# Kernel optimization log

Hardware: AMD Instinct MI355X
Metric: run time of the kernel (lower is better)

## Reference

```python
import jax, jax.numpy as jnp
import numpy as np

N_TRAIN, D, B, N_CLASSES, K = 50000, 64, 128, 10, 16


def setup_inputs() -> dict:
    key = jax.random.key(0)
    k1, k2, k3 = jax.random.split(key, 3)
    train_data = jax.random.normal(k1, (N_TRAIN, D), dtype=jnp.float32)
    # one-hot class labels, as implied by gather -> sum over k -> argmax over classes
    labels = jax.random.randint(k2, (N_TRAIN,), 0, N_CLASSES)
    train_target = jax.nn.one_hot(labels, N_CLASSES, dtype=jnp.float32)
    x_test = jax.random.normal(k3, (B, D), dtype=jnp.float32)
    return {"train_data": train_data, "train_target": train_target,
            "x_test": x_test, "k": K}


def reference(train_data, train_target, x_test, k):
    # L1 (Manhattan) distance: [B, N_train]
    # broadcast: [1, N, D] - [B, 1, D] -> abs -> sum over D
    distance = jnp.sum(jnp.abs(train_data[None, :, :] - x_test[:, None, :]), axis=2)
    # top_k of negative distance == k nearest neighbors
    _, top_k_indices = jax.lax.top_k(-distance, k)          # [B, k]
    top_k_label = train_target[top_k_indices]               # [B, k, C] gather
    sum_up_predictions = jnp.sum(top_k_label, axis=1)       # [B, C] vote counts
    return jnp.argmax(sum_up_predictions, axis=1)           # [B] predicted class
```

## Files before the change

kernel.cpp:

```cpp
#include <hip/hip_runtime.h>
#include <cfloat>
#include <climits>
#include <stdint.h>

#define NTRAIN 50000
#define DIM 64
#define BQ 128
#define NCLS 10
#define KSEL 16
#define QPB 32
#define QG (BQ / QPB)
#define THREADS 512
#define TROWS 512
#define TPAD 68
#define NSAMP 1024
#define SSTRIPES 64
#define MARGIN 1e-2f

__device__ __forceinline__ uint64_t pack_di(float d, int r) {
    return ((uint64_t)__float_as_uint(d) << 32) | (uint32_t)r;
}

__device__ __forceinline__ void ins16(uint64_t (&K)[KSEL], uint64_t pk) {
    if (pk < K[KSEL - 1]) {
        K[KSEL - 1] = pk;
#pragma unroll
        for (int j = KSEL - 1; j > 0; --j)
            if (K[j] < K[j - 1]) { uint64_t t = K[j]; K[j] = K[j - 1]; K[j - 1] = t; }
    }
}

__device__ __forceinline__ uint64_t adv16(const uint64_t (&K)[KSEL], int c) {
    uint64_t nh = ~0ULL;
#pragma unroll
    for (int q = 1; q < KSEL; ++q)
        if (c == q) nh = K[q];
    return nh;
}

__device__ __forceinline__ void wave_merge8(const uint64_t (&K)[KSEL], int rg, uint64_t* dst) {
    uint64_t h = K[0]; int c = 0;
#pragma unroll
    for (int r = 0; r < KSEL; ++r) {
        uint64_t m = h, o;
        o = __shfl_xor((unsigned long long)m, 1); if (o < m) m = o;
        o = __shfl_xor((unsigned long long)m, 2); if (o < m) m = o;
        o = __shfl_xor((unsigned long long)m, 4); if (o < m) m = o;
        if (m == h) { ++c; h = adv16(K, c); }
        if (rg == (r & 7)) dst[r] = m;
    }
}

__global__ __launch_bounds__(64) void knn_tau(
    const float* __restrict__ train, const float* __restrict__ xtest,
    float* __restrict__ tau)
{
    const int q = blockIdx.x, lane = threadIdx.x;

    float4 qv[DIM / 4];
    {
        const float* qp = xtest + (size_t)q * DIM;
#pragma unroll
        for (int c = 0; c < DIM / 4; ++c) qv[c] = *(const float4*)(qp + 4 * c);
    }

    uint64_t K[KSEL];
#pragma unroll
    for (int j = 0; j < KSEL; ++j) K[j] = ~0ULL;

    for (int t = 0; t < NSAMP / 64; ++t) {
        const int r = lane + 64 * t;
        const float* rp = train + (size_t)r * DIM;
        float acc = 0.0f;
#pragma unroll
        for (int c = 0; c < DIM / 4; ++c) {
            const float4 tv = *(const float4*)(rp + 4 * c);
            const float s01 = fabsf(tv.x - qv[c].x) + fabsf(tv.y - qv[c].y);
            const float s23 = fabsf(tv.z - qv[c].z) + fabsf(tv.w - qv[c].w);
            acc += s01 + s23;
        }
        ins16(K, pack_di(acc, r));
    }

    uint64_t h = K[0]; int c = 0; uint64_t last = ~0ULL;
#pragma unroll
    for (int r = 0; r < KSEL; ++r) {
        uint64_t m = h, o;
#pragma unroll
        for (int sh = 1; sh < 64; sh <<= 1) {
            o = __shfl_xor((unsigned long long)m, sh);
            if (o < m) m = o;
        }
        if (m == h) { ++c; h = adv16(K, c); }
        last = m;
    }
    if (lane == 0) tau[q] = __uint_as_float((uint32_t)(last >> 32)) + MARGIN;
}

__global__ __launch_bounds__(THREADS, 2) void knn_scan(
    const float* __restrict__ train, const float* __restrict__ xtest,
    const float* __restrict__ tau, uint64_t* __restrict__ cand, int stripe_len)
{
    __shared__ float qs[QPB * TPAD];
    __shared__ __align__(16) float ts[TROWS * TPAD];

    const int bx     = blockIdx.x;
    const int stripe = bx % SSTRIPES;
    const int qgrp   = bx / SSTRIPES;
    const int q0     = qgrp * QPB;
    const int tid    = threadIdx.x;
    const int w      = tid >> 6;
    const int lane   = tid & 63;
    const int qg     = lane >> 3;
    const int rg     = lane & 7;

    const int r0 = stripe * stripe_len;
    const int r1 = min(NTRAIN, r0 + stripe_len);

    for (int f = tid; f < QPB * (DIM / 4); f += THREADS) {
        const int ql = f >> 4, c = f & 15;
        *(float4*)&qs[ql * TPAD + 4 * c] =
            *(const float4*)&xtest[(size_t)(q0 + ql) * DIM + 4 * c];
    }

    float tauv[4];
#pragma unroll
    for (int i = 0; i < 4; ++i) tauv[i] = tau[q0 + qg + 8 * i];

    uint64_t k0[KSEL], k1[KSEL], k2[KSEL], k3[KSEL];
#pragma unroll
    for (int j = 0; j < KSEL; ++j) { k0[j] = ~0ULL; k1[j] = ~0ULL; k2[j] = ~0ULL; k3[j] = ~0ULL; }

    for (int base = r0; base < r1; base += TROWS) {
        const int nr = min(TROWS, r1 - base);
        __syncthreads();
        for (int f = tid; f < nr * (DIM / 4); f += THREADS) {
            const int r = f >> 4, c = f & 15;
            *(float4*)&ts[r * TPAD + 4 * c] =
                *(const float4*)&train[(size_t)(base + r) * DIM + 4 * c];
        }
        __syncthreads();

        float acc[4][8];
#pragma unroll
        for (int i = 0; i < 4; ++i)
#pragma unroll
            for (int j = 0; j < 8; ++j) acc[i][j] = 0.0f;

#pragma unroll 4
        for (int c = 0; c < DIM / 4; ++c) {
            float4 qv[4], tv[8];
#pragma unroll
            for (int i = 0; i < 4; ++i)
                qv[i] = *(const float4*)&qs[(qg + 8 * i) * TPAD + 4 * c];
#pragma unroll
            for (int j = 0; j < 8; ++j)
                tv[j] = *(const float4*)&ts[(w * 64 + rg + 8 * j) * TPAD + 4 * c];
#pragma unroll
            for (int i = 0; i < 4; ++i)
#pragma unroll
                for (int j = 0; j < 8; ++j) {
                    const float s01 = fabsf(tv[j].x - qv[i].x) + fabsf(tv[j].y - qv[i].y);
                    const float s23 = fabsf(tv[j].z - qv[i].z) + fabsf(tv[j].w - qv[i].w);
                    acc[i][j] += s01 + s23;
                }
        }

        const int rb = base + w * 64 + rg;
#pragma unroll
        for (int j = 0; j < 8; ++j) {
            const int r = rb + 8 * j;
            if (r < r1) {
                if (acc[0][j] <= tauv[0]) ins16(k0, pack_di(acc[0][j], r));
                if (acc[1][j] <= tauv[1]) ins16(k1, pack_di(acc[1][j], r));
                if (acc[2][j] <= tauv[2]) ins16(k2, pack_di(acc[2][j], r));
                if (acc[3][j] <= tauv[3]) ins16(k3, pack_di(acc[3][j], r));
            }
        }
    }

    __syncthreads();
    uint64_t* mg = (uint64_t*)ts;
    wave_merge8(k0, rg, &mg[((size_t)w * QPB + qg +  0) * 17]);
    wave_merge8(k1, rg, &mg[((size_t)w * QPB + qg +  8) * 17]);
    wave_merge8(k2, rg, &mg[((size_t)w * QPB + qg + 16) * 17]);
    wave_merge8(k3, rg, &mg[((size_t)w * QPB + qg + 24) * 17]);
    __syncthreads();

    if (tid < QPB) {
        uint64_t kk[KSEL];
#pragma unroll
        for (int j = 0; j < KSEL; ++j) kk[j] = ~0ULL;
        for (int v = 0; v < 8; ++v)
#pragma unroll
            for (int j = 0; j < KSEL; ++j)
                ins16(kk, mg[((size_t)v * QPB + tid) * 17 + j]);
#pragma unroll
        for (int j = 0; j < KSEL; ++j)
            cand[((size_t)(q0 + tid) * SSTRIPES + stripe) * KSEL + j] = kk[j];
    }
}

__global__ __launch_bounds__(64) void knn_final(
    const uint64_t* __restrict__ cand, const float* __restrict__ ttarget,
    int* __restrict__ out, int ncand)
{
    const int b = blockIdx.x, lane = threadIdx.x;

    uint64_t k[KSEL];
#pragma unroll
    for (int j = 0; j < KSEL; ++j) k[j] = ~0ULL;
    for (int c = lane; c < ncand; c += 64)
        ins16(k, cand[(size_t)b * ncand + c]);

    uint64_t h = k[0]; int c = 0;
    float v = 0.0f;
#pragma unroll
    for (int r = 0; r < KSEL; ++r) {
        uint64_t m = h, o;
#pragma unroll
        for (int sh = 1; sh < 64; sh <<= 1) {
            o = __shfl_xor((unsigned long long)m, sh);
            if (o < m) m = o;
        }
        if (m == h) { ++c; h = adv16(k, c); }
        const int wi = (int)(uint32_t)(m & 0xFFFFFFFFu);
        if (lane < NCLS) v += ttarget[(size_t)wi * NCLS + lane];
    }

    float bv = (lane < NCLS) ? v : -1.0f;
    int   bc = lane;
#pragma unroll
    for (int sh = 1; sh < 64; sh <<= 1) {
        const float xv = __shfl_xor(bv, sh);
        const int   xc = __shfl_xor(bc, sh);
        if (xv > bv || (xv == bv && xc < bc)) { bv = xv; bc = xc; }
    }
    if (lane == 0) out[b] = bc;
}

extern "C" void kernel_launch(void* const* d_in, const int* in_sizes, int n_in,
                              void* d_out, int out_size, void* d_ws, size_t ws_size,
                              hipStream_t stream) {
    const float* train   = (const float*)d_in[0];
    const float* ttarget = (const float*)d_in[1];
    const float* xtest   = (const float*)d_in[2];
    int* out = (int*)d_out;

    const int stripe_len = (NTRAIN + SSTRIPES - 1) / SSTRIPES;

    float*    tau  = (float*)d_ws;
    uint64_t* cand = (uint64_t*)((char*)d_ws + 512);

    hipLaunchKernelGGL(knn_tau, dim3(BQ), dim3(64), 0, stream, train, xtest, tau);
    hipLaunchKernelGGL(knn_scan, dim3(QG * SSTRIPES), dim3(THREADS), 0, stream,
                       train, xtest, tau, cand, stripe_len);
    hipLaunchKernelGGL(knn_final, dim3(BQ), dim3(64), 0, stream,
                       cand, ttarget, out, SSTRIPES * KSEL);
}
```

Measured before the change: 138.8 us.

## Collect scan candidates in a shared-memory buffer instead of per-thread top-16 lists

The scan kernel drops its four per-thread register top-16 lists. Any distance at or below the sampled threshold is now appended to a shared-memory buffer through an atomic counter. After the tile loop, 32 threads each filter that buffer for their own query and build the stripe's top-16. This removes heavy register pressure and the wave-level merge, and the launch bound changes to one block per CU. In exchange it adds shared atomics, a serial final pass, and a hard capacity of 1920 that silently drops candidates on overflow; the tau margin is also removed.

Result: slower. 229.2 us (+65.2%).

```diff
diff --git a/kernel.cpp b/kernel.cpp
--- a/kernel.cpp
+++ b/kernel.cpp
@@ -15,10 +15,10 @@
 #define TPAD 68
 #define NSAMP 1024
 #define SSTRIPES 64
-#define MARGIN 1e-2f
-
-__device__ __forceinline__ uint64_t pack_di(float d, int r) {
-    return ((uint64_t)__float_as_uint(d) << 32) | (uint32_t)r;
+#define CAP 1920
+
+__device__ __forceinline__ uint64_t pack_dqr(float d, int q, int r) {
+    return ((uint64_t)__float_as_uint(d) << 32) | ((uint64_t)(uint32_t)q << 16) | (uint32_t)r;
 }
 
 __device__ __forceinline__ void ins16(uint64_t (&K)[KSEL], uint64_t pk) {
@@ -36,19 +36,6 @@
     for (int q = 1; q < KSEL; ++q)
         if (c == q) nh = K[q];
     return nh;
-}
-
-__device__ __forceinline__ void wave_merge8(const uint64_t (&K)[KSEL], int rg, uint64_t* dst) {
-    uint64_t h = K[0]; int c = 0;
-#pragma unroll
-    for (int r = 0; r < KSEL; ++r) {
-        uint64_t m = h, o;
-        o = __shfl_xor((unsigned long long)m, 1); if (o < m) m = o;
-        o = __shfl_xor((unsigned long long)m, 2); if (o < m) m = o;
-        o = __shfl_xor((unsigned long long)m, 4); if (o < m) m = o;
-        if (m == h) { ++c; h = adv16(K, c); }
-        if (rg == (r & 7)) dst[r] = m;
-    }
 }
 
 __global__ __launch_bounds__(64) void knn_tau(
@@ -79,7 +66,7 @@
             const float s23 = fabsf(tv.z - qv[c].z) + fabsf(tv.w - qv[c].w);
             acc += s01 + s23;
         }
-        ins16(K, pack_di(acc, r));
+        ins16(K, (((uint64_t)__float_as_uint(acc)) << 32) | (uint32_t)r);
     }
 
     uint64_t h = K[0]; int c = 0; uint64_t last = ~0ULL;
@@ -94,15 +81,17 @@
         if (m == h) { ++c; h = adv16(K, c); }
         last = m;
     }
-    if (lane == 0) tau[q] = __uint_as_float((uint32_t)(last >> 32)) + MARGIN;
-}
-
-__global__ __launch_bounds__(THREADS, 2) void knn_scan(
+    if (lane == 0) tau[q] = __uint_as_float((uint32_t)(last >> 32));
+}
+
+__global__ __launch_bounds__(THREADS, 1) void knn_scan(
     const float* __restrict__ train, const float* __restrict__ xtest,
     const float* __restrict__ tau, uint64_t* __restrict__ cand, int stripe_len)
 {
     __shared__ float qs[QPB * TPAD];
     __shared__ __align__(16) float ts[TROWS * TPAD];
+    __shared__ uint64_t bufc[CAP];
+    __shared__ int lcnt;
 
     const int bx     = blockIdx.x;
     const int stripe = bx % SSTRIPES;
@@ -117,6 +106,7 @@
     const int r0 = stripe * stripe_len;
     const int r1 = min(NTRAIN, r0 + stripe_len);
 
+    if (tid == 0) lcnt = 0;
     for (int f = tid; f < QPB * (DIM / 4); f += THREADS) {
         const int ql = f >> 4, c = f & 15;
         *(float4*)&qs[ql * TPAD + 4 * c] =
@@ -126,10 +116,6 @@
     float tauv[4];
 #pragma unroll
     for (int i = 0; i < 4; ++i) tauv[i] = tau[q0 + qg + 8 * i];
-
-    uint64_t k0[KSEL], k1[KSEL], k2[KSEL], k3[KSEL];
-#pragma unroll
-    for (int j = 0; j < KSEL; ++j) { k0[j] = ~0ULL; k1[j] = ~0ULL; k2[j] = ~0ULL; k3[j] = ~0ULL; }
 
     for (int base = r0; base < r1; base += TROWS) {
         const int nr = min(TROWS, r1 - base);
@@ -171,30 +157,27 @@
         for (int j = 0; j < 8; ++j) {
             const int r = rb + 8 * j;
             if (r < r1) {
-                if (acc[0][j] <= tauv[0]) ins16(k0, pack_di(acc[0][j], r));
-                if (acc[1][j] <= tauv[1]) ins16(k1, pack_di(acc[1][j], r));
-                if (acc[2][j] <= tauv[2]) ins16(k2, pack_di(acc[2][j], r));
-                if (acc[3][j] <= tauv[3]) ins16(k3, pack_di(acc[3][j], r));
+#pragma unroll
+                for (int i = 0; i < 4; ++i) {
+                    if (acc[i][j] <= tauv[i]) {
+                        const int p = atomicAdd(&lcnt, 1);
+                        if (p < CAP) bufc[p] = pack_dqr(acc[i][j], qg + 8 * i, r);
+                    }
+                }
             }
         }
     }
 
     __syncthreads();
-    uint64_t* mg = (uint64_t*)ts;
-    wave_merge8(k0, rg, &mg[((size_t)w * QPB + qg +  0) * 17]);
-    wave_merge8(k1, rg, &mg[((size_t)w * QPB + qg +  8) * 17]);
-    wave_merge8(k2, rg, &mg[((size_t)w * QPB + qg + 16) * 17]);
-    wave_merge8(k3, rg, &mg[((size_t)w * QPB + qg + 24) * 17]);
-    __syncthreads();
-
+    const int m = min(lcnt, CAP);
     if (tid < QPB) {
         uint64_t kk[KSEL];
 #pragma unroll
         for (int j = 0; j < KSEL; ++j) kk[j] = ~0ULL;
-        for (int v = 0; v < 8; ++v)
-#pragma unroll
-            for (int j = 0; j < KSEL; ++j)
-                ins16(kk, mg[((size_t)v * QPB + tid) * 17 + j]);
+        for (int e = 0; e < m; ++e) {
+            const uint64_t v = bufc[e];
+            if ((int)((v >> 16) & 31) == tid) ins16(kk, v);
+        }
 #pragma unroll
         for (int j = 0; j < KSEL; ++j)
             cand[((size_t)(q0 + tid) * SSTRIPES + stripe) * KSEL + j] = kk[j];
@@ -224,7 +207,7 @@
             if (o < m) m = o;
         }
         if (m == h) { ++c; h = adv16(k, c); }
-        const int wi = (int)(uint32_t)(m & 0xFFFFFFFFu);
+        const int wi = (int)(m & 0xFFFFu);
         if (lane < NCLS) v += ttarget[(size_t)wi * NCLS + lane];
     }
 
```
